# Kernel optimization log

Measured on AMD Instinct MI355X. Metric: run time of the kernel, lower is better.

## Reference

```python
import jax, jax.numpy as jnp
import numpy as np

FEATURE_SCALE = 0.25  # cfg.feature_scale
G = 4                 # deformable/offset groups
K = 3                 # deform kernel size
KK = K * K
PAD = 1


def conv2d(x, w, b=None):
    y = jax.lax.conv_general_dilated(x, w, (1, 1), ((PAD, PAD), (PAD, PAD)),
                                     dimension_numbers=('NCHW', 'OIHW', 'NCHW'))
    return y if b is None else y + b[None, :, None, None]


def bilinear_upsample_ac(x, fs):
    # F.interpolate(mode='bilinear', align_corners=True, scale_factor=fs)
    b, c, H, W = x.shape
    Ho, Wo = H * fs, W * fs
    sy = jnp.arange(Ho, dtype=x.dtype) * ((H - 1) / (Ho - 1))
    sx = jnp.arange(Wo, dtype=x.dtype) * ((W - 1) / (Wo - 1))
    y0 = jnp.clip(jnp.floor(sy).astype(jnp.int32), 0, H - 2)
    x0 = jnp.clip(jnp.floor(sx).astype(jnp.int32), 0, W - 2)
    wy = (sy - y0)[None, None, :, None]
    wx = (sx - x0)[None, None, None, :]
    rows = x[:, :, y0, :] * (1 - wy) + x[:, :, y0 + 1, :] * wy
    return rows[:, :, :, x0] * (1 - wx) + rows[:, :, :, x0 + 1] * wx


def deform_conv(x, offset, mask, w):
    # torchvision.ops.deform_conv2d, stride 1, pad 1, weight groups = 1,
    # offset/mask groups = G. offset layout: (b, G*KK*2, H, W), (dy, dx) pairs.
    b, C, H, W = x.shape
    Cg = C // G
    off = offset.reshape(b, G, KK, 2, H, W)
    ii = (jnp.arange(KK) // K).reshape(1, 1, KK, 1, 1).astype(x.dtype)
    jj = (jnp.arange(KK) % K).reshape(1, 1, KK, 1, 1).astype(x.dtype)
    ys = jnp.arange(H, dtype=x.dtype).reshape(1, 1, 1, H, 1)
    xs = jnp.arange(W, dtype=x.dtype).reshape(1, 1, 1, 1, W)
    py = ys - PAD + ii + off[:, :, :, 0]   # (b,G,KK,H,W)
    px = xs - PAD + jj + off[:, :, :, 1]
    xt = x.reshape(b, G, Cg, H, W).transpose(0, 1, 3, 4, 2)  # (b,G,H,W,Cg)
    y0f = jnp.floor(py)
    x0f = jnp.floor(px)
    wy = py - y0f
    wx = px - x0f
    y0 = y0f.astype(jnp.int32)
    x0 = x0f.astype(jnp.int32)
    bi = jnp.arange(b).reshape(b, 1, 1, 1, 1)
    gi = jnp.arange(G).reshape(1, G, 1, 1, 1)

    def corner(yi, xi, wgt):
        valid = ((yi >= 0) & (yi < H) & (xi >= 0) & (xi < W)).astype(x.dtype)
        v = xt[bi, gi, jnp.clip(yi, 0, H - 1), jnp.clip(xi, 0, W - 1)]  # (b,G,KK,H,W,Cg)
        return v * (wgt * valid)[..., None]

    s = (corner(y0, x0, (1 - wy) * (1 - wx)) + corner(y0, x0 + 1, (1 - wy) * wx)
         + corner(y0 + 1, x0, wy * (1 - wx)) + corner(y0 + 1, x0 + 1, wy * wx))
    s = s * mask.reshape(b, G, KK, H, W)[..., None]
    wr = w.reshape(w.shape[0], G, Cg, KK)
    return jnp.einsum('bgkhwc,ogck->bohw', s, wr)


def _align(sou_list, ref_list, params):
    cat_feat, offset_vs = [], []
    for i in (3, 2, 1):
        sou, ref = sou_list[i - 1], ref_list[i - 1]
        b, C, H, W = sou.shape
        Cg = C // G
        off_w, off_b, mod_w, mod_b, reg_w = params[i]
        off_in = jnp.concatenate([sou.reshape(b, G, Cg, H, W),
                                  ref.reshape(b, G, Cg, H, W)], axis=2)
        off_in = off_in.reshape(b * G, 2 * Cg, H, W)
        offset = conv2d(off_in, off_w, off_b).reshape(b, G * 2 * KK, H, W)
        rng = min(H, W) * 0.5 / 2
        offset_map = rng * 2 * jax.nn.sigmoid(offset) - rng
        modulator = 2.0 * jax.nn.sigmoid(conv2d(sou, mod_w, mod_b))
        feat = deform_conv(sou, offset_map, modulator, reg_w)
        fs = int(1 // (FEATURE_SCALE / 2 ** (i - 1)))
        oy = jnp.mean(offset_map[:, 0::2], axis=1, keepdims=True)
        ox = jnp.mean(offset_map[:, 1::2], axis=1, keepdims=True)
        ov = bilinear_upsample_ac(jnp.concatenate([oy, ox], axis=1), fs) * fs
        cat_feat.append(feat)
        offset_vs.append(ov)
    return tuple(cat_feat) + tuple(offset_vs)


def setup_inputs() -> dict:
    key = jax.random.key(0)
    ks = jax.random.split(key, 32)
    d = {}
    shapes = {1: (2, 64, 128, 128), 2: (2, 64, 64, 64), 3: (2, 64, 32, 32)}
    k = 0
    for i in (1, 2, 3):
        d[f'sou{i}'] = jax.random.normal(ks[k], shapes[i], jnp.float32); k += 1
        d[f'ref{i}'] = jax.random.normal(ks[k], shapes[i], jnp.float32); k += 1
    Cg = 64 // G
    for i in (1, 2, 3):
        d[f'off_w{i}'] = jax.random.normal(ks[k], (2 * KK, 2 * Cg, K, K), jnp.float32) * 0.05; k += 1
        d[f'off_b{i}'] = jax.random.normal(ks[k], (2 * KK,), jnp.float32) * 0.05; k += 1
        d[f'mod_w{i}'] = jax.random.normal(ks[k], (G * KK, 64, K, K), jnp.float32) * 0.05; k += 1
        d[f'mod_b{i}'] = jax.random.normal(ks[k], (G * KK,), jnp.float32) * 0.05; k += 1
        d[f'reg_w{i}'] = jax.random.normal(ks[k], (64, 64, K, K), jnp.float32) * 0.05; k += 1
    return d


def reference(sou1, sou2, sou3, ref1, ref2, ref3,
              off_w1, off_b1, mod_w1, mod_b1, reg_w1,
              off_w2, off_b2, mod_w2, mod_b2, reg_w2,
              off_w3, off_b3, mod_w3, mod_b3, reg_w3):
    params = {1: (off_w1, off_b1, mod_w1, mod_b1, reg_w1),
              2: (off_w2, off_b2, mod_w2, mod_b2, reg_w2),
              3: (off_w3, off_b3, mod_w3, mod_b3, reg_w3)}
    return _align([sou1, sou2, sou3], [ref1, ref2, ref3], params)
```

## Files before the change

### kernel.cpp

```cpp
#include <hip/hip_runtime.h>

typedef __attribute__((ext_vector_type(8))) short short8;
typedef __attribute__((ext_vector_type(4))) float f32x4;

__device__ __forceinline__ float sigmoidf_(float x) { return 1.f / (1.f + __expf(-x)); }
__device__ __forceinline__ unsigned bf16rne(float x) {
    unsigned b = __float_as_uint(x);
    return (b + 0x7FFFu + ((b >> 16) & 1u)) >> 16;
}


struct P {
    const float *sou0, *sou1, *sou2;
    const float *ref0, *ref1, *ref2;
    const float *ob0, *ob1, *ob2;
    const float *mb0, *mb1, *mb2;
    float* out;
    float* ws;
};

union U {
    uint4 u4; int4 i4; short8 s8; f32x4 f4;
};

__global__ __launch_bounds__(256) void repack_all(
    const float* __restrict__ ow0, const float* __restrict__ mw0, const float* __restrict__ rw0,
    const float* __restrict__ ow1, const float* __restrict__ mw1, const float* __restrict__ rw1,
    const float* __restrict__ ow2, const float* __restrict__ mw2, const float* __restrict__ rw2,
    float* __restrict__ dst) {
    const int lvl = blockIdx.y;
    const float* ow = lvl == 0 ? ow0 : (lvl == 1 ? ow1 : ow2);
    const float* mw = lvl == 0 ? mw0 : (lvl == 1 ? mw1 : mw2);
    const float* rw = lvl == 0 ? rw0 : (lvl == 1 ? rw1 : rw2);
    unsigned* d = (unsigned*)(dst + lvl * 62784);
    int i = blockIdx.x * 256 + threadIdx.x;
    if (i < 18432) {
        int jw = i & 3;
        int lane = (i >> 2) & 63;
        int t3 = i >> 8;
        int ks = t3 % 18, wvu = t3 / 18;
        int o = wvu * 16 + (lane & 15);
        int c0 = ks * 32 + (lane >> 4) * 8 + 2 * jw;
        int g0 = c0 / 144, r0 = c0 % 144;
        int c1 = c0 + 1;
        int g1 = c1 / 144, r1 = c1 % 144;
        float w0 = rw[o * 576 + (g0 * 16 + (r0 & 15)) * 9 + (r0 >> 4)];
        float w1 = rw[o * 576 + (g1 * 16 + (r1 & 15)) * 9 + (r1 >> 4)];
        d[i] = bf16rne(w0) | (bf16rne(w1) << 16);
    } else if (i < 23552) {
        int o2 = i - 18432;
        int jw = o2 & 3;
        int lane = (o2 >> 2) & 63;
        int t2 = o2 >> 8;
        int nt = t2 & 1;
        int hk = t2 >> 1;
        int ks = hk % 5, h = hk / 5;
        int n = nt * 16 + (lane & 15);
        int K = ks * 32 + (lane >> 4) * 8 + 2 * jw;
        int tap = K >> 4, ch = K & 15;
        bool ok = (n < 18) && (tap < 9);
        float w0 = ok ? ow[n * 288 + (h * 16 + ch) * 9 + tap] : 0.f;
        float w1 = ok ? ow[n * 288 + (h * 16 + ch + 1) * 9 + tap] : 0.f;
        d[36864 + o2] = bf16rne(w0) | (bf16rne(w1) << 16);
    } else if (i < 37376) {
        int o3 = i - 23552;
        int jw = o3 & 3;
        int lane = (o3 >> 2) & 63;
        int t3 = o3 >> 8;
        int nt = t3 % 3, tc = t3 / 3;
        int tap = tc >> 1, c = tc & 1;
        int n = nt * 16 + (lane & 15);
        int ic0 = c * 32 + (lane >> 4) * 8 + 2 * jw;
        float w0 = (n < 36) ? mw[n * 576 + ic0 * 9 + tap] : 0.f;
        float w1 = (n < 36) ? mw[n * 576 + (ic0 + 1) * 9 + tap] : 0.f;
        d[41984 + o3] = bf16rne(w0) | (bf16rne(w1) << 16);
    }
}

__global__ __launch_bounds__(256) void k1_prep(P p) {
    __shared__ __align__(16) char smem[28512];
    const int t = blockIdx.x;
    float* ws = p.ws;
    const int tid = threadIdx.x;

    int lvl, j;
    if (t < 512) { lvl = 0; j = t; }
    else if (t < 640) { lvl = 1; j = t - 512; }
    else { lvl = 2; j = t - 640; }
    const int logW = 7 - lvl;
    const int W = 1 << logW, H = W, HW = H * W;
    const int nper = 256 >> (2 * lvl);
    const int qb = j % nper, b = j / nper;
    const int q0 = qb * 64;
    const int hlo = q0 >> logW;
    const int xlo = q0 & (W - 1);
    const int cols = (W >= 64) ? 66 : 34;
    const int rcTot = (W >= 64) ? 198 : 136;
    const float* sou = lvl == 0 ? p.sou0 : (lvl == 1 ? p.sou1 : p.sou2);
    const float* ref = lvl == 0 ? p.ref0 : (lvl == 1 ? p.ref1 : p.ref2);
    const float* base_s = sou + (size_t)b * 64 * HW;
    const float* base_r = ref + (size_t)b * 64 * HW;
    unsigned* ldsW = (unsigned*)smem;
    const bool sact = tid < rcTot;
    const int srow = tid / cols, scol = tid - srow * cols;
    const int grow = hlo - 1 + srow, gcol = xlo - 1 + scol;
    const bool inb = sact && grow >= 0 && grow < H && gcol >= 0 && gcol < W;
    const size_t goff = inb ? ((size_t)grow * W + gcol) : 0;

#pragma unroll
    for (int c8 = 0; c8 < 8; ++c8) {
        const float* p0 = base_s + (size_t)(c8 * 8) * HW;
        float v[8];
#pragma unroll
        for (int jj = 0; jj < 8; ++jj) v[jj] = inb ? p0[(size_t)jj * HW + goff] : 0.f;
        if (sact) {
            uint4 wv;
            wv.x = bf16rne(v[0]) | (bf16rne(v[1]) << 16);
            wv.y = bf16rne(v[2]) | (bf16rne(v[3]) << 16);
            wv.z = bf16rne(v[4]) | (bf16rne(v[5]) << 16);
            wv.w = bf16rne(v[6]) | (bf16rne(v[7]) << 16);
            *(uint4*)&ldsW[tid * 36 + c8 * 4] = wv;
        }
    }
    __syncthreads();

    unsigned* XTb = (unsigned*)(ws + 4919232) +
                    (lvl == 0 ? 0 : (lvl == 1 ? 1048576 : 1310720));
#pragma unroll
    for (int u = 0; u < 2; ++u) {
        const int idx = tid * 2 + u;
        const int px = idx >> 3, gh = idx & 7;
        const int g = gh >> 1, half = gh & 1;
        const int rc = ((px >> logW) + 1) * cols + (px & (W - 1)) + 1;
        uint4 v = *(const uint4*)&ldsW[rc * 36 + g * 8 + half * 4];
        *(uint4*)(XTb + ((size_t)(b * 4 + g) * HW + q0 + px) * 8 + half * 4) = v;
    }

    const int wvu = __builtin_amdgcn_readfirstlane(tid >> 6);
    const int lane = tid & 63, quad = lane >> 4, lo16 = lane & 15;
    const int qg = q0 + wvu * 16 + lo16;
    const int rowB = (qg >> logW) - hlo;
    const int colB = (qg & (W - 1)) - xlo;
    const unsigned short* ldsS = (const unsigned short*)smem;
    const unsigned* WREPu = (const unsigned*)(ws + 4730880 + lvl * 62784);
    const unsigned* WBO2 = WREPu + 36864;
    const unsigned* WBM = WREPu + 41984;

    f32x4 accM[3], accO[4][2];
#pragma unroll
    for (int nt = 0; nt < 3; ++nt) accM[nt] = (f32x4){0.f, 0.f, 0.f, 0.f};
#pragma unroll
    for (int g = 0; g < 4; ++g)
#pragma unroll
        for (int nt = 0; nt < 2; ++nt) accO[g][nt] = (f32x4){0.f, 0.f, 0.f, 0.f};

#pragma unroll
    for (int tap = 0; tap < 9; ++tap) {
        const int ky = tap / 3, kx = tap - ky * 3;
        const int rc = (rowB + ky) * cols + colB + kx;
#pragma unroll
        for (int c = 0; c < 2; ++c) {
            U au; au.s8 = *(const short8*)&ldsS[rc * 72 + c * 32 + quad * 8];
#pragma unroll
            for (int nt = 0; nt < 3; ++nt) {
                U bu;
                bu.u4 = *(const uint4*)(WBM + (((tap * 2 + c) * 3 + nt) * 64 + lane) * 4);
                accM[nt] = __builtin_amdgcn_mfma_f32_16x16x32_bf16(au.s8, bu.s8, accM[nt], 0, 0, 0);
            }
        }
    }
#pragma unroll
    for (int ks = 0; ks < 5; ++ks) {
        const int Kbase = ks * 32 + quad * 8;
        const int tap = min(Kbase >> 4, 8);
        const int ky = tap / 3, kx = tap - ky * 3;
        const int rc = (rowB + ky) * cols + colB + kx;
        const int choff = Kbase & 15;
#pragma unroll
        for (int g = 0; g < 4; ++g) {
            U au; au.s8 = *(const short8*)&ldsS[rc * 72 + g * 16 + choff];
#pragma unroll
            for (int nt = 0; nt < 2; ++nt) {
                U bu;
                bu.u4 = *(const uint4*)(WBO2 + ((ks * 2 + nt) * 64 + lane) * 4);
                accO[g][nt] =
                    __builtin_amdgcn_mfma_f32_16x16x32_bf16(au.s8, bu.s8, accO[g][nt], 0, 0, 0);
            }
        }
    }
    __syncthreads();

#pragma unroll
    for (int c8 = 0; c8 < 8; ++c8) {
        const float* p0 = base_r + (size_t)(c8 * 8) * HW;
        float v[8];
#pragma unroll
        for (int jj = 0; jj < 8; ++jj) v[jj] = inb ? p0[(size_t)jj * HW + goff] : 0.f;
        if (sact) {
            uint4 wv;
            wv.x = bf16rne(v[0]) | (bf16rne(v[1]) << 16);
            wv.y = bf16rne(v[2]) | (bf16rne(v[3]) << 16);
            wv.z = bf16rne(v[4]) | (bf16rne(v[5]) << 16);
            wv.w = bf16rne(v[6]) | (bf16rne(v[7]) << 16);
            *(uint4*)&ldsW[tid * 36 + c8 * 4] = wv;
        }
    }
    __syncthreads();

#pragma unroll
    for (int ks = 0; ks < 5; ++ks) {
        const int Kbase = ks * 32 + quad * 8;
        const int tap = min(Kbase >> 4, 8);
        const int ky = tap / 3, kx = tap - ky * 3;
        const int rc = (rowB + ky) * cols + colB + kx;
        const int choff = Kbase & 15;
#pragma unroll
        for (int g = 0; g < 4; ++g) {
            U au; au.s8 = *(const short8*)&ldsS[rc * 72 + g * 16 + choff];
#pragma unroll
            for (int nt = 0; nt < 2; ++nt) {
                U bu;
                bu.u4 = *(const uint4*)(WBO2 + (((5 + ks) * 2 + nt) * 64 + lane) * 4);
                accO[g][nt] =
                    __builtin_amdgcn_mfma_f32_16x16x32_bf16(au.s8, bu.s8, accO[g][nt], 0, 0, 0);
            }
        }
    }

    {
        const float* bias = lvl == 0 ? p.mb0 : (lvl == 1 ? p.mb1 : p.mb2);
        float* MOD = ws + (lvl == 0 ? 3096576 : (lvl == 1 ? 4276224 : 4571136));
#pragma unroll
        for (int nt = 0; nt < 3; ++nt) {
            const int o = nt * 16 + lo16;
            if (o < 36) {
                const float bb = bias[o];
                float* op = MOD + (size_t)(b * 36 + o) * HW + q0 + wvu * 16 + quad * 4;
#pragma unroll
                for (int rg = 0; rg < 4; ++rg)
                    op[rg] = 2.f * sigmoidf_(accM[nt][rg] + bb);
            }
        }
    }
    {
        const float* bias = lvl == 0 ? p.ob0 : (lvl == 1 ? p.ob1 : p.ob2);
        float* OFFM = ws + (lvl == 0 ? 0 : (lvl == 1 ? 2359296 : 2949120));
        const float rng = 0.25f * (float)H;
#pragma unroll
        for (int g = 0; g < 4; ++g)
#pragma unroll
            for (int nt = 0; nt < 2; ++nt) {
                const int o = nt * 16 + lo16;
                if (o < 18) {
                    const float bb = bias[o];
                    float* op = OFFM + (size_t)(b * 72 + g * 18 + o) * HW + q0 + wvu * 16 + quad * 4;
#pragma unroll
                    for (int rg = 0; rg < 4; ++rg)
                        op[rg] = rng * (2.f * sigmoidf_(accO[g][nt][rg] + bb) - 1.f);
                }
            }
    }
}

__global__ __launch_bounds__(256) void k2_fused(P p) {
    __shared__ unsigned lds[96 * 33];
    const int t = blockIdx.x;
    float* ws = p.ws;
    const int tid = threadIdx.x;
    if (t < 1344) {
        int lvl, j;
        if (t < 1024) { lvl = 0; j = t; }
        else if (t < 1280) { lvl = 1; j = t - 1024; }
        else { lvl = 2; j = t - 1280; }
        const int logW = 7 - lvl;
        const int W = 1 << logW, H = W, HW = H * W;
        const int nper = 512 >> (2 * lvl);
        const int qb = j % nper, b = j / nper;
        const int q0 = qb * 32;
        const float* OFFM = ws + (lvl == 0 ? 0 : (lvl == 1 ? 2359296 : 2949120));
        const float* MOD = ws + (lvl == 0 ? 3096576 : (lvl == 1 ? 4276224 : 4571136));
        const unsigned* XTb = (const unsigned*)(ws + 4919232) +
                              (lvl == 0 ? 0 : (lvl == 1 ? 1048576 : 1310720));
        const unsigned* WB = (const unsigned*)(ws + 4730880 + lvl * 62784);
        float* outp = p.out + (lvl == 0 ? 655360 : (lvl == 1 ? 131072 : 0));
        const int wvu = __builtin_amdgcn_readfirstlane(tid >> 6);
        const int lane = tid & 63, quad = lane >> 4, lo16 = lane & 15;
        f32x4 acc[2];
        acc[0] = (f32x4){0.f, 0.f, 0.f, 0.f};
        acc[1] = (f32x4){0.f, 0.f, 0.f, 0.f};
        for (int c = 0; c < 3; ++c) {
            if (c) __syncthreads();
#pragma unroll
            for (int it = 0; it < 2; ++it) {
                const int task = it * 256 + tid;
                if (task < 384) {
                    const int gkl = task >> 5, px = task & 31;
                    const int gk = c * 12 + gkl;
                    const int g = gk / 9, k = gk - g * 9;
                    const int q = q0 + px;
                    const int h = q >> logW, xp = q & (W - 1);
                    const int ky = k / 3, kx = k - ky * 3;
                    float dy = OFFM[(size_t)(b * 72 + g * 18 + 2 * k) * HW + q];
                    float dx = OFFM[(size_t)(b * 72 + g * 18 + 2 * k + 1) * HW + q];
                    float m = MOD[(size_t)(b * 36 + g * 9 + k) * HW + q];
                    float py = (float)(h - 1 + ky) + dy;
                    float pxx = (float)(xp - 1 + kx) + dx;
                    float y0f = floorf(py), x0f = floorf(pxx);
                    float wy = py - y0f, wx = pxx - x0f;
                    int y0 = (int)y0f, x0 = (int)x0f;
                    const unsigned* xg = XTb + (size_t)(b * 4 + g) * HW * 8;
                    float s[16];
#pragma unroll
                    for (int cc = 0; cc < 16; ++cc) s[cc] = 0.f;
#pragma unroll
                    for (int cor = 0; cor < 4; ++cor) {
                        int yy = y0 + (cor >> 1), xx = x0 + (cor & 1);
                        float cw = ((cor >> 1) ? wy : 1.f - wy) * ((cor & 1) ? wx : 1.f - wx);
                        cw = (yy >= 0 && yy < H && xx >= 0 && xx < W) ? cw * m : 0.f;
                        int yc = min(max(yy, 0), H - 1), xc = min(max(xx, 0), W - 1);
                        const uint4* cp = (const uint4*)(xg + (size_t)((yc << logW) + xc) * 8);
                        unsigned cbuf[8];
                        *(uint4*)&cbuf[0] = cp[0];
                        *(uint4*)&cbuf[4] = cp[1];
#pragma unroll
                        for (int pr = 0; pr < 8; ++pr) {
                            float lo = __uint_as_float(cbuf[pr] << 16);
                            float hi = __uint_as_float(cbuf[pr] & 0xFFFF0000u);
                            s[2 * pr] = fmaf(cw, lo, s[2 * pr]);
                            s[2 * pr + 1] = fmaf(cw, hi, s[2 * pr + 1]);
                        }
                    }
#pragma unroll
                    for (int pr = 0; pr < 8; ++pr)
                        lds[(gkl * 8 + pr) * 33 + px] =
                            bf16rne(s[2 * pr]) | (bf16rne(s[2 * pr + 1]) << 16);
                }
            }
            __syncthreads();
            uint4 bfr[6];
#pragma unroll
            for (int k6 = 0; k6 < 6; ++k6)
                bfr[k6] = *(const uint4*)(WB + (((wvu * 18 + c * 6 + k6) * 64 + lane) << 2));
#pragma unroll
            for (int k6 = 0; k6 < 6; ++k6) {
                const int rb = k6 * 16 + quad * 4;
                U bu; bu.u4 = bfr[k6];
#pragma unroll
                for (int mt = 0; mt < 2; ++mt) {
                    const int px = mt * 16 + lo16;
                    U au;
                    au.i4.x = (int)lds[(rb + 0) * 33 + px];
                    au.i4.y = (int)lds[(rb + 1) * 33 + px];
                    au.i4.z = (int)lds[(rb + 2) * 33 + px];
                    au.i4.w = (int)lds[(rb + 3) * 33 + px];
                    acc[mt] = __builtin_amdgcn_mfma_f32_16x16x32_bf16(au.s8, bu.s8, acc[mt], 0, 0, 0);
                }
            }
        }
        float* op = outp + (size_t)(b * 64 + wvu * 16 + lo16) * HW + q0;
#pragma unroll
        for (int mt = 0; mt < 2; ++mt)
#pragma unroll
            for (int rg = 0; rg < 4; ++rg)
                op[mt * 16 + quad * 4 + rg] = acc[mt][rg];
    } else {
        int i = t - 1344;
        int lvl, j;
        if (i < 128) { lvl = 0; j = i; }
        else if (i < 160) { lvl = 1; j = i - 128; }
        else { lvl = 2; j = i - 160; }
        const int HW = 16384 >> (2 * lvl);
        const int nper = 64 >> (2 * lvl);
        const int qb = j % nper, b = j / nper;
        const float* OFFM = ws + (lvl == 0 ? 0 : (lvl == 1 ? 2359296 : 2949120));
        float* MEAN = ws + (lvl == 0 ? 4644864 : (lvl == 1 ? 4710400 : 4726784));
        const int q = qb * 256 + tid;
        const float* pp = OFFM + (size_t)b * 72 * HW + q;
        float sy = 0.f, sx = 0.f;
#pragma unroll
        for (int u = 0; u < 36; ++u) {
            sy += pp[(size_t)(2 * u) * HW];
            sx += pp[(size_t)(2 * u + 1) * HW];
        }
        MEAN[(size_t)(b * 2) * HW + q] = sy * (1.f / 36.f);
        MEAN[(size_t)(b * 2 + 1) * HW + q] = sx * (1.f / 36.f);
    }
}

__global__ __launch_bounds__(256) void k3_up(P p) {
    float* ws = p.ws;
    int flat = ((int)blockIdx.x * 256 + (int)threadIdx.x) * 4;
    int lvl = flat >> 20;
    int r = flat & 1048575;
    int b = r >> 19, c = (r >> 18) & 1;
    int pix = r & 262143;
    int yo = pix >> 9, xo = pix & 511;
    const int H = 128 >> lvl, W = H;
    const float* MEAN = ws + (lvl == 0 ? 4644864 : (lvl == 1 ? 4710400 : 4726784));
    const float* m = MEAN + (size_t)(b * 2 + c) * H * W;
    float* o = p.out + (lvl == 0 ? 4849664 : (lvl == 1 ? 3801088 : 2752512)) +
               ((size_t)(b * 2 + c) * 512 + yo) * 512 + xo;
    const float fs = (float)(4 << lvl);
    const float sc = (float)(H - 1) * (1.f / 511.f);
    float sy = yo * sc;
    int y0 = min((int)sy, H - 2);
    float wy = sy - (float)y0;
    float rr[4];
#pragma unroll
    for (int u = 0; u < 4; ++u) {
        float sx = (float)(xo + u) * sc;
        int x0 = min((int)sx, W - 2);
        float wx = sx - (float)x0;
        float v00 = m[y0 * W + x0], v01 = m[y0 * W + x0 + 1];
        float v10 = m[(y0 + 1) * W + x0], v11 = m[(y0 + 1) * W + x0 + 1];
        float r0 = v00 * (1.f - wy) + v10 * wy;
        float r1 = v01 * (1.f - wy) + v11 * wy;
        rr[u] = (r0 * (1.f - wx) + r1 * wx) * fs;
    }
    *(float4*)o = make_float4(rr[0], rr[1], rr[2], rr[3]);
}

extern "C" void kernel_launch(void* const* d_in, const int* in_sizes, int n_in,
                              void* d_out, int out_size, void* d_ws, size_t ws_size,
                              hipStream_t stream) {
    const float* fin[21];
    for (int i = 0; i < 21; ++i) fin[i] = (const float*)d_in[i];
    P p;
    if (in_sizes[1] == in_sizes[0]) {
        p.sou0 = fin[0]; p.ref0 = fin[1];
        p.sou1 = fin[2]; p.ref1 = fin[3];
        p.sou2 = fin[4]; p.ref2 = fin[5];
    } else {
        p.sou0 = fin[0]; p.sou1 = fin[1]; p.sou2 = fin[2];
        p.ref0 = fin[3]; p.ref1 = fin[4]; p.ref2 = fin[5];
    }
    p.ob0 = fin[7]; p.mb0 = fin[9];
    p.ob1 = fin[12]; p.mb1 = fin[14];
    p.ob2 = fin[17]; p.mb2 = fin[19];
    p.out = (float*)d_out;
    p.ws = (float*)d_ws;

    repack_all<<<dim3(146, 3), 256, 0, stream>>>(
        fin[6], fin[8], fin[10], fin[11], fin[13], fin[15], fin[16], fin[18], fin[20],
        p.ws + 4730880);
    k1_prep<<<dim3(672), 256, 0, stream>>>(p);
    k2_fused<<<dim3(1512), 256, 0, stream>>>(p);
    k3_up<<<dim3(3072), 256, 0, stream>>>(p);
}
```

Baseline: 176.9 us.

## Fuse offset-mean into prep, merge upsample into k2, vectorize LDS and stores

The prep kernel now stages the sou and ref tiles into two separate LDS buffers up front, which removes a barrier-separated reload, and computes the per-pixel offset mean with warp shuffles right after writing the offsets. This removes the separate mean pass that re-read all 72 offset channels. The upsample kernel is folded into k2's grid, saving one launch. k2's LDS layout is transposed so the A fragments come from single 16-byte reads, and the output stores are vectorized. Doubling k1's LDS may lower its occupancy, and the upsample blocks now run in the same grid as the heavy deform blocks.

```diff
diff --git a/kernel.cpp b/kernel.cpp
--- a/kernel.cpp
+++ b/kernel.cpp
@@ -78,7 +78,7 @@
 }
 
 __global__ __launch_bounds__(256) void k1_prep(P p) {
-    __shared__ __align__(16) char smem[28512];
+    __shared__ __align__(16) char smem[57024];
     const int t = blockIdx.x;
     float* ws = p.ws;
     const int tid = threadIdx.x;
@@ -101,6 +101,7 @@
     const float* base_s = sou + (size_t)b * 64 * HW;
     const float* base_r = ref + (size_t)b * 64 * HW;
     unsigned* ldsW = (unsigned*)smem;
+    unsigned* ldsW2 = (unsigned*)(smem + 28512);
     const bool sact = tid < rcTot;
     const int srow = tid / cols, scol = tid - srow * cols;
     const int grow = hlo - 1 + srow, gcol = xlo - 1 + scol;
@@ -122,6 +123,21 @@
             *(uint4*)&ldsW[tid * 36 + c8 * 4] = wv;
         }
     }
+#pragma unroll
+    for (int c8 = 0; c8 < 8; ++c8) {
+        const float* p0 = base_r + (size_t)(c8 * 8) * HW;
+        float v[8];
+#pragma unroll
+        for (int jj = 0; jj < 8; ++jj) v[jj] = inb ? p0[(size_t)jj * HW + goff] : 0.f;
+        if (sact) {
+            uint4 wv;
+            wv.x = bf16rne(v[0]) | (bf16rne(v[1]) << 16);
+            wv.y = bf16rne(v[2]) | (bf16rne(v[3]) << 16);
+            wv.z = bf16rne(v[4]) | (bf16rne(v[5]) << 16);
+            wv.w = bf16rne(v[6]) | (bf16rne(v[7]) << 16);
+            *(uint4*)&ldsW2[tid * 36 + c8 * 4] = wv;
+        }
+    }
     __syncthreads();
 
     unsigned* XTb = (unsigned*)(ws + 4919232) +
@@ -142,6 +158,7 @@
     const int rowB = (qg >> logW) - hlo;
     const int colB = (qg & (W - 1)) - xlo;
     const unsigned short* ldsS = (const unsigned short*)smem;
+    const unsigned short* ldsS2 = (const unsigned short*)(smem + 28512);
     const unsigned* WREPu = (const unsigned*)(ws + 4730880 + lvl * 62784);
     const unsigned* WBO2 = WREPu + 36864;
     const unsigned* WBM = WREPu + 41984;
@@ -188,25 +205,6 @@
             }
         }
     }
-    __syncthreads();
-
-#pragma unroll
-    for (int c8 = 0; c8 < 8; ++c8) {
-        const float* p0 = base_r + (size_t)(c8 * 8) * HW;
-        float v[8];
-#pragma unroll
-        for (int jj = 0; jj < 8; ++jj) v[jj] = inb ? p0[(size_t)jj * HW + goff] : 0.f;
-        if (sact) {
-            uint4 wv;
-            wv.x = bf16rne(v[0]) | (bf16rne(v[1]) << 16);
-            wv.y = bf16rne(v[2]) | (bf16rne(v[3]) << 16);
-            wv.z = bf16rne(v[4]) | (bf16rne(v[5]) << 16);
-            wv.w = bf16rne(v[6]) | (bf16rne(v[7]) << 16);
-            *(uint4*)&ldsW[tid * 36 + c8 * 4] = wv;
-        }
-    }
-    __syncthreads();
-
 #pragma unroll
     for (int ks = 0; ks < 5; ++ks) {
         const int Kbase = ks * 32 + quad * 8;
@@ -216,7 +214,7 @@
         const int choff = Kbase & 15;
 #pragma unroll
         for (int g = 0; g < 4; ++g) {
-            U au; au.s8 = *(const short8*)&ldsS[rc * 72 + g * 16 + choff];
+            U au; au.s8 = *(const short8*)&ldsS2[rc * 72 + g * 16 + choff];
 #pragma unroll
             for (int nt = 0; nt < 2; ++nt) {
                 U bu;
@@ -236,9 +234,10 @@
             if (o < 36) {
                 const float bb = bias[o];
                 float* op = MOD + (size_t)(b * 36 + o) * HW + q0 + wvu * 16 + quad * 4;
-#pragma unroll
-                for (int rg = 0; rg < 4; ++rg)
-                    op[rg] = 2.f * sigmoidf_(accM[nt][rg] + bb);
+                *(float4*)op = make_float4(2.f * sigmoidf_(accM[nt][0] + bb),
+                                           2.f * sigmoidf_(accM[nt][1] + bb),
+                                           2.f * sigmoidf_(accM[nt][2] + bb),
+                                           2.f * sigmoidf_(accM[nt][3] + bb));
             }
         }
     }
@@ -246,6 +245,7 @@
         const float* bias = lvl == 0 ? p.ob0 : (lvl == 1 ? p.ob1 : p.ob2);
         float* OFFM = ws + (lvl == 0 ? 0 : (lvl == 1 ? 2359296 : 2949120));
         const float rng = 0.25f * (float)H;
+        float macc[4] = {0.f, 0.f, 0.f, 0.f};
 #pragma unroll
         for (int g = 0; g < 4; ++g)
 #pragma unroll
@@ -253,17 +253,45 @@
                 const int o = nt * 16 + lo16;
                 if (o < 18) {
                     const float bb = bias[o];
+                    float ovv[4];
+#pragma unroll
+                    for (int rg = 0; rg < 4; ++rg)
+                        ovv[rg] = rng * (2.f * sigmoidf_(accO[g][nt][rg] + bb) - 1.f);
                     float* op = OFFM + (size_t)(b * 72 + g * 18 + o) * HW + q0 + wvu * 16 + quad * 4;
-#pragma unroll
-                    for (int rg = 0; rg < 4; ++rg)
-                        op[rg] = rng * (2.f * sigmoidf_(accO[g][nt][rg] + bb) - 1.f);
+                    *(float4*)op = make_float4(ovv[0], ovv[1], ovv[2], ovv[3]);
+#pragma unroll
+                    for (int rg = 0; rg < 4; ++rg) macc[rg] += ovv[rg];
                 }
             }
+        const bool odd = (lo16 & 1) != 0;
+        float my[4], mx[4];
+#pragma unroll
+        for (int rg = 0; rg < 4; ++rg) {
+            my[rg] = odd ? 0.f : macc[rg];
+            mx[rg] = odd ? macc[rg] : 0.f;
+        }
+#pragma unroll
+        for (int m = 1; m < 16; m <<= 1) {
+#pragma unroll
+            for (int rg = 0; rg < 4; ++rg) {
+                my[rg] += __shfl_xor(my[rg], m);
+                mx[rg] += __shfl_xor(mx[rg], m);
+            }
+        }
+        if (lo16 == 0) {
+            float* MEAN = ws + (lvl == 0 ? 4644864 : (lvl == 1 ? 4710400 : 4726784));
+            const int pxb = q0 + wvu * 16 + quad * 4;
+            const float inv = 1.f / 36.f;
+            *(float4*)(MEAN + (size_t)(b * 2) * HW + pxb) =
+                make_float4(my[0] * inv, my[1] * inv, my[2] * inv, my[3] * inv);
+            *(float4*)(MEAN + (size_t)(b * 2 + 1) * HW + pxb) =
+                make_float4(mx[0] * inv, mx[1] * inv, mx[2] * inv, mx[3] * inv);
+        }
     }
 }
 
 __global__ __launch_bounds__(256) void k2_fused(P p) {
-    __shared__ unsigned lds[96 * 33];
+    __shared__ __align__(16) unsigned lds[32 * 100];
     const int t = blockIdx.x;
     float* ws = p.ws;
     const int tid = threadIdx.x;
@@ -330,10 +358,18 @@
                             s[2 * pr + 1] = fmaf(cw, hi, s[2 * pr + 1]);
                         }
                     }
-#pragma unroll
-                    for (int pr = 0; pr < 8; ++pr)
-                        lds[(gkl * 8 + pr) * 33 + px] =
-                            bf16rne(s[2 * pr]) | (bf16rne(s[2 * pr + 1]) << 16);
+                    unsigned* dp = &lds[px * 100 + gkl * 8];
+                    uint4 w0, w1;
+                    w0.x = bf16rne(s[0]) | (bf16rne(s[1]) << 16);
+                    w0.y = bf16rne(s[2]) | (bf16rne(s[3]) << 16);
+                    w0.z = bf16rne(s[4]) | (bf16rne(s[5]) << 16);
+                    w0.w = bf16rne(s[6]) | (bf16rne(s[7]) << 16);
+                    w1.x = bf16rne(s[8]) | (bf16rne(s[9]) << 16);
+                    w1.y = bf16rne(s[10]) | (bf16rne(s[11]) << 16);
+                    w1.z = bf16rne(s[12]) | (bf16rne(s[13]) << 16);
+                    w1.w = bf16rne(s[14]) | (bf16rne(s[15]) << 16);
+                    *(uint4*)dp = w0;
+                    *(uint4*)(dp + 4) = w1;
                 }
             }
             __syncthreads();
@@ -343,16 +379,12 @@
                 bfr[k6] = *(const uint4*)(WB + (((wvu * 18 + c * 6 + k6) * 64 + lane) << 2));
 #pragma unroll
             for (int k6 = 0; k6 < 6; ++k6) {
-                const int rb = k6 * 16 + quad * 4;
                 U bu; bu.u4 = bfr[k6];
 #pragma unroll
                 for (int mt = 0; mt < 2; ++mt) {
                     const int px = mt * 16 + lo16;
                     U au;
-                    au.i4.x = (int)lds[(rb + 0) * 33 + px];
-                    au.i4.y = (int)lds[(rb + 1) * 33 + px];
-                    au.i4.z = (int)lds[(rb + 2) * 33 + px];
-                    au.i4.w = (int)lds[(rb + 3) * 33 + px];
+                    au.u4 = *(const uint4*)&lds[px * 100 + k6 * 16 + quad * 4];
                     acc[mt] = __builtin_amdgcn_mfma_f32_16x16x32_bf16(au.s8, bu.s8, acc[mt], 0, 0, 0);
                 }
             }
@@ -364,60 +396,36 @@
             for (int rg = 0; rg < 4; ++rg)
                 op[mt * 16 + quad * 4 + rg] = acc[mt][rg];
     } else {
-        int i = t - 1344;
-        int lvl, j;
-        if (i < 128) { lvl = 0; j = i; }
-        else if (i < 160) { lvl = 1; j = i - 128; }
-        else { lvl = 2; j = i - 160; }
-        const int HW = 16384 >> (2 * lvl);
-        const int nper = 64 >> (2 * lvl);
-        const int qb = j % nper, b = j / nper;
-        const float* OFFM = ws + (lvl == 0 ? 0 : (lvl == 1 ? 2359296 : 2949120));
-        float* MEAN = ws + (lvl == 0 ? 4644864 : (lvl == 1 ? 4710400 : 4726784));
-        const int q = qb * 256 + tid;
-        const float* pp = OFFM + (size_t)b * 72 * HW + q;
-        float sy = 0.f, sx = 0.f;
-#pragma unroll
-        for (int u = 0; u < 36; ++u) {
-            sy += pp[(size_t)(2 * u) * HW];
-            sx += pp[(size_t)(2 * u + 1) * HW];
-        }
-        MEAN[(size_t)(b * 2) * HW + q] = sy * (1.f / 36.f);
-        MEAN[(size_t)(b * 2 + 1) * HW + q] = sx * (1.f / 36.f);
-    }
-}
-
-__global__ __launch_bounds__(256) void k3_up(P p) {
-    float* ws = p.ws;
-    int flat = ((int)blockIdx.x * 256 + (int)threadIdx.x) * 4;
-    int lvl = flat >> 20;
-    int r = flat & 1048575;
-    int b = r >> 19, c = (r >> 18) & 1;
-    int pix = r & 262143;
-    int yo = pix >> 9, xo = pix & 511;
-    const int H = 128 >> lvl, W = H;
-    const float* MEAN = ws + (lvl == 0 ? 4644864 : (lvl == 1 ? 4710400 : 4726784));
-    const float* m = MEAN + (size_t)(b * 2 + c) * H * W;
-    float* o = p.out + (lvl == 0 ? 4849664 : (lvl == 1 ? 3801088 : 2752512)) +
-               ((size_t)(b * 2 + c) * 512 + yo) * 512 + xo;
-    const float fs = (float)(4 << lvl);
-    const float sc = (float)(H - 1) * (1.f / 511.f);
-    float sy = yo * sc;
-    int y0 = min((int)sy, H - 2);
-    float wy = sy - (float)y0;
-    float rr[4];
-#pragma unroll
-    for (int u = 0; u < 4; ++u) {
-        float sx = (float)(xo + u) * sc;
-        int x0 = min((int)sx, W - 2);
-        float wx = sx - (float)x0;
-        float v00 = m[y0 * W + x0], v01 = m[y0 * W + x0 + 1];
-        float v10 = m[(y0 + 1) * W + x0], v11 = m[(y0 + 1) * W + x0 + 1];
-        float r0 = v00 * (1.f - wy) + v10 * wy;
-        float r1 = v01 * (1.f - wy) + v11 * wy;
-        rr[u] = (r0 * (1.f - wx) + r1 * wx) * fs;
-    }
-    *(float4*)o = make_float4(rr[0], rr[1], rr[2], rr[3]);
+        int flat = ((t - 1344) * 256 + tid) * 4;
+        int lvl = flat >> 20;
+        int r = flat & 1048575;
+        int b = r >> 19, c = (r >> 18) & 1;
+        int pix = r & 262143;
+        int yo = pix >> 9, xo = pix & 511;
+        const int H = 128 >> lvl, W = H;
+        const float* MEAN = ws + (lvl == 0 ? 4644864 : (lvl == 1 ? 4710400 : 4726784));
+        const float* m = MEAN + (size_t)(b * 2 + c) * H * W;
+        float* o = p.out + (lvl == 0 ? 4849664 : (lvl == 1 ? 3801088 : 2752512)) +
+                   ((size_t)(b * 2 + c) * 512 + yo) * 512 + xo;
+        const float fs = (float)(4 << lvl);
+        const float sc = (float)(H - 1) * (1.f / 511.f);
+        float sy = yo * sc;
+        int y0 = min((int)sy, H - 2);
+        float wy = sy - (float)y0;
+        float rr[4];
+#pragma unroll
+        for (int u = 0; u < 4; ++u) {
+            float sx = (float)(xo + u) * sc;
+            int x0 = min((int)sx, W - 2);
+            float wx = sx - (float)x0;
+            float v00 = m[y0 * W + x0], v01 = m[y0 * W + x0 + 1];
+            float v10 = m[(y0 + 1) * W + x0], v11 = m[(y0 + 1) * W + x0 + 1];
+            float r0 = v00 * (1.f - wy) + v10 * wy;
+            float r1 = v01 * (1.f - wy) + v11 * wy;
+            rr[u] = (r0 * (1.f - wx) + r1 * wx) * fs;
+        }
+        *(float4*)o = make_float4(rr[0], rr[1], rr[2], rr[3]);
+    }
 }
 
 extern "C" void kernel_launch(void* const* d_in, const int* in_sizes, int n_in,
@@ -444,6 +452,5 @@
         fin[6], fin[8], fin[10], fin[11], fin[13], fin[15], fin[16], fin[18], fin[20],
         p.ws + 4730880);
     k1_prep<<<dim3(672), 256, 0, stream>>>(p);
-    k2_fused<<<dim3(1512), 256, 0, stream>>>(p);
-    k3_up<<<dim3(3072), 256, 0, stream>>>(p);
+    k2_fused<<<dim3(4416), 256, 0, stream>>>(p);
 }
```

Result: slower. 196.4 us (+11.0%).
